# Kernel optimization log

Hardware: AMD Instinct MI355X
Metric: run time of the kernel (lower is better)

## Reference

```python
import jax, jax.numpy as jnp
import numpy as np

H, W, D, C = 32, 16, 16, 4
NUM_ITERS = 2
THETA_GAMMA = 3.0   # spatial (position-only) kernel bandwidth
THETA_ALPHA = 8.0   # bilateral position bandwidth
THETA_BETA = 0.5    # bilateral color bandwidth


def _attn(feats, q):
    # Gaussian-kernel attention: softmax_j(-0.5 * ||f_i - f_j||^2) @ q
    # feats: [N, F], q: [N, C] -> [N, C]
    sq = jnp.sum(feats * feats, axis=-1)
    logits = feats @ feats.T - 0.5 * (sq[:, None] + sq[None, :])  # [N, N]
    return jax.nn.softmax(logits, axis=-1) @ q


def setup_inputs() -> dict:
    key = jax.random.key(0)
    k1, k2 = jax.random.split(key)
    unaries = jax.random.normal(k1, (1, H, W, D, C), dtype=jnp.float32)
    rgb = jax.random.normal(k2, (1, H, W, D, 3), dtype=jnp.float32)
    eye = jnp.eye(C, dtype=jnp.float32)
    return {
        "unaries": unaries,
        "rgb": rgb,
        "spatial_ker_weights": eye,          # _diagonal_initializer
        "bilateral_ker_weights": eye,        # _diagonal_initializer
        "compatibility_matrix": -eye,        # _potts_model_initializer
    }


def reference(unaries, rgb, spatial_ker_weights, bilateral_ker_weights, compatibility_matrix):
    N = H * W * D
    # positions start at 1 as in tf.range(1, h+1)
    grids = jnp.meshgrid(jnp.arange(1, H + 1), jnp.arange(1, W + 1), jnp.arange(1, D + 1), indexing='ij')
    pos = jnp.stack(grids, axis=-1).astype(jnp.float32).reshape(N, 3)
    rgb_flat = rgb.reshape(N, 3)
    spatial_feats = pos / THETA_GAMMA                                             # [N, 3]
    bilateral_feats = jnp.concatenate([pos / THETA_ALPHA, rgb_flat / THETA_BETA], axis=-1)  # [N, 6]

    u = unaries.reshape(N, C)
    q = u
    for _ in range(NUM_ITERS):
        sm = jax.nn.softmax(q, axis=-1)                         # [N, C]
        spatial_out = _attn(spatial_feats, sm)                  # [N, C]
        bilateral_out = _attn(bilateral_feats, sm)              # [N, C]
        # message_passing = SK @ spatial + BK @ bilateral (class-space matmul)
        message = spatial_out @ spatial_ker_weights.T + bilateral_out @ bilateral_ker_weights.T
        pairwise = message @ compatibility_matrix.T             # [N, C]
        q = u + pairwise
    return q.reshape(unaries.shape)
```

## Files before the change

kernel.cpp:

```cpp
#include <hip/hip_runtime.h>


#define HH 32
#define WW 16
#define DDD 16
#define NN (HH * WW * DDD)
#define KS 16
#define JCH (NN / KS)
#define CONVB 32
#define ITILB (NN / 64)
#define GB2 (ITILB * KS)
#define L2E 1.4426950408889634f
#define C18 (L2E / 18.0f)
#define SQL2E 1.2011224087864498f
#define SB (SQL2E / 8.0f)
#define SC (SQL2E / 0.5f)

#if __has_builtin(__builtin_amdgcn_exp2f)
#define EXP2(x) __builtin_amdgcn_exp2f(x)
#else
#define EXP2(x) exp2f(x)
#endif

typedef __attribute__((ext_vector_type(8))) short bf16x8;
typedef __attribute__((ext_vector_type(4))) float f32x4;
#define MFMA16 __builtin_amdgcn_mfma_f32_16x16x32_bf16

__device__ __forceinline__ unsigned short f2bf(float x) {
    unsigned int u = __float_as_uint(x);
    return (unsigned short)((u + 0x7FFFu + ((u >> 16) & 1u)) >> 16);
}
__device__ __forceinline__ float bf2f(unsigned short b) {
    return __uint_as_float(((unsigned int)b) << 16);
}
__device__ __forceinline__ unsigned int pk(unsigned short a, unsigned short b) {
    return (unsigned int)a | ((unsigned int)b << 16);
}

__global__ __launch_bounds__(256) void prep(
    const float* __restrict__ u, const float* __restrict__ rgb,
    unsigned short* __restrict__ fq, unsigned short* __restrict__ fk,
    float* __restrict__ sm0, unsigned short* __restrict__ smT0)
{
    int i = blockIdx.x * 256 + threadIdx.x;
    int h = i >> 8, r = i & 255, w = r >> 4, d = r & 15;
    float f[6];
    f[0] = (float)(h + 1) * SB;
    f[1] = (float)(w + 1) * SB;
    f[2] = (float)(d + 1) * SB;
    f[3] = rgb[3 * i + 0] * SC;
    f[4] = rgb[3 * i + 1] * SC;
    f[5] = rgb[3 * i + 2] * SC;
    float nh = -0.5f * (f[0]*f[0] + f[1]*f[1] + f[2]*f[2] +
                        f[3]*f[3] + f[4]*f[4] + f[5]*f[5]);
    unsigned short hi[7], lo[7];
    #pragma unroll
    for (int k = 0; k < 6; ++k) {
        hi[k] = f2bf(f[k]);
        lo[k] = f2bf(f[k] - bf2f(hi[k]));
    }
    hi[6] = f2bf(nh);
    lo[6] = f2bf(nh - bf2f(hi[6]));
    const unsigned short one = 0x3F80;

    uint4* q4 = (uint4*)(fq + (size_t)i * 32);
    uint4* k4 = (uint4*)(fk + (size_t)i * 32);
    q4[0] = make_uint4(pk(hi[0],hi[1]), pk(hi[2],hi[3]), pk(hi[4],hi[5]), pk(hi[6],one));
    q4[1] = make_uint4(pk(lo[0],lo[1]), pk(lo[2],lo[3]), pk(lo[4],lo[5]), pk(lo[6],0));
    q4[2] = make_uint4(pk(hi[0],hi[1]), pk(hi[2],hi[3]), pk(hi[4],hi[5]), pk(0,one));
    q4[3] = make_uint4(0, 0, 0, 0);
    k4[0] = make_uint4(pk(hi[0],hi[1]), pk(hi[2],hi[3]), pk(hi[4],hi[5]), pk(one,hi[6]));
    k4[1] = make_uint4(pk(hi[0],hi[1]), pk(hi[2],hi[3]), pk(hi[4],hi[5]), pk(one,0));
    k4[2] = make_uint4(pk(lo[0],lo[1]), pk(lo[2],lo[3]), pk(lo[4],lo[5]), pk(0,lo[6]));
    k4[3] = make_uint4(0, 0, 0, 0);

    float4 q = ((const float4*)u)[i];
    float m = fmaxf(fmaxf(q.x, q.y), fmaxf(q.z, q.w));
    float e0 = EXP2((q.x - m) * L2E), e1 = EXP2((q.y - m) * L2E);
    float e2 = EXP2((q.z - m) * L2E), e3 = EXP2((q.w - m) * L2E);
    float rs = 1.0f / (e0 + e1 + e2 + e3);
    float s0 = e0 * rs, s1 = e1 * rs, s2 = e2 * rs, s3 = e3 * rs;
    ((float4*)sm0)[i] = make_float4(s0, s1, s2, s3);
    smT0[0 * NN + i] = f2bf(s0);
    smT0[1 * NN + i] = f2bf(s1);
    smT0[2 * NN + i] = f2bf(s2);
    smT0[3 * NN + i] = f2bf(s3);
}

__global__ __launch_bounds__(256, 8) void fused(
    const float* __restrict__ sm,
    const unsigned short* __restrict__ smT,
    const unsigned short* __restrict__ fq,
    const unsigned short* __restrict__ fk,
    float* __restrict__ part,
    float* __restrict__ tmp)
{
    __shared__ float lds[2048];
    int tid = threadIdx.x;

    if (blockIdx.x < GB2) {
        int b = blockIdx.x;
        int ibk = b >> 4;
        int kc = b & (KS - 1);
        int wv = tid >> 6, lane = tid & 63;
        int lm = lane & 15, lg = lane >> 4;
        int i0 = ibk * 64 + wv * 16;
        int j0 = kc * JCH;

        const bf16x8* FQ = (const bf16x8*)fq;
        const bf16x8* FK = (const bf16x8*)fk;
        bf16x8 Bf = FK[(size_t)(i0 + lm) * 4 + lg];
        const unsigned short* smc = smT + (size_t)(lm & 3) * NN;

        unsigned int* P = (unsigned int*)lds + wv * 320;
        f32x4 acc = {0.f, 0.f, 0.f, 0.f};
        const f32x4 zro = {0.f, 0.f, 0.f, 0.f};

        #pragma unroll 2
        for (int s = 0; s < JCH / 32; ++s) {
            int js = j0 + s * 32;
            bf16x8 A0 = FQ[(size_t)(js + lm) * 4 + lg];
            bf16x8 A1 = FQ[(size_t)(js + 16 + lm) * 4 + lg];
            f32x4 S0 = MFMA16(A0, Bf, zro, 0, 0, 0);
            f32x4 S1 = MFMA16(A1, Bf, zro, 0, 0, 0);
            uint2 w0, w1;
            w0.x = pk(f2bf(EXP2(S0[0])), f2bf(EXP2(S0[1])));
            w0.y = pk(f2bf(EXP2(S0[2])), f2bf(EXP2(S0[3])));
            w1.x = pk(f2bf(EXP2(S1[0])), f2bf(EXP2(S1[1])));
            w1.y = pk(f2bf(EXP2(S1[2])), f2bf(EXP2(S1[3])));
            *(uint2*)(P + lm * 20 + 2 * lg)     = w0;
            *(uint2*)(P + lm * 20 + 2 * lg + 8) = w1;
            bf16x8 Pf = *(const bf16x8*)(P + lm * 20 + 4 * lg);
            bf16x8 Sf = *(const bf16x8*)(smc + js + 8 * lg);
            acc = MFMA16(Pf, Sf, acc, 0, 0, 0);
        }
        if (lm < 4) {
            float* pp = part + (size_t)kc * (NN * 4);
            #pragma unroll
            for (int r = 0; r < 4; ++r)
                pp[(size_t)(i0 + 4 * lg + r) * 4 + lm] = acc[r];
        }
    } else {
        int h = blockIdx.x - GB2;
        int s = tid;
        int i = h * 256 + s;

        float* A = lds;
        float* B = lds + 1024;
        *((float4*)(A + 4 * s)) = ((const float4*)sm)[i];
        __syncthreads();

        int w = s >> 4, d = s & 15;
        float t0 = 0, t1 = 0, t2 = 0, t3 = 0;
        #pragma unroll
        for (int dp = 0; dp < DDD; ++dp) {
            float dd = (float)(d - dp);
            float k = EXP2(-dd * dd * C18);
            const float4 v = *((const float4*)(A + 4 * (w * 16 + dp)));
            t0 = fmaf(k, v.x, t0); t1 = fmaf(k, v.y, t1);
            t2 = fmaf(k, v.z, t2); t3 = fmaf(k, v.w, t3);
        }
        *((float4*)(B + 4 * s)) = make_float4(t0, t1, t2, t3);
        __syncthreads();

        float u0 = 0, u1 = 0, u2 = 0, u3 = 0;
        #pragma unroll
        for (int wp = 0; wp < WW; ++wp) {
            float dw = (float)(w - wp);
            float k = EXP2(-dw * dw * C18);
            const float4 v = *((const float4*)(B + 4 * (wp * 16 + d)));
            u0 = fmaf(k, v.x, u0); u1 = fmaf(k, v.y, u1);
            u2 = fmaf(k, v.z, u2); u3 = fmaf(k, v.w, u3);
        }
        *((float4*)(tmp + 4 * i)) = make_float4(u0, u1, u2, u3);
    }
}

__global__ __launch_bounds__(256) void reduce_finish(
    const float* __restrict__ part,
    const float* __restrict__ tmp,
    const float* __restrict__ u,
    const float* __restrict__ sk, const float* __restrict__ bk,
    const float* __restrict__ cm,
    float* __restrict__ qout,
    float* __restrict__ smout,
    unsigned short* __restrict__ smTout)
{
    int tid = threadIdx.x;
    int q = tid >> 6;
    int lane = tid & 63;
    int idx = blockIdx.x * 64 + lane;

    float bl = 0.0f;
    #pragma unroll
    for (int k = 0; k < KS / 4; ++k)
        bl += part[(size_t)(q * (KS / 4) + k) * (NN * 4) + idx];

    int i = idx >> 2;
    int h = i >> 8;
    int scid = idx & 1023;
    float sp = 0.0f;
    #pragma unroll
    for (int k = 0; k < 8; ++k) {
        int hp = q * 8 + k;
        float dh = (float)(h - hp);
        float kk = EXP2(-dh * dh * C18);
        sp = fmaf(kk, tmp[hp * 1024 + scid], sp);
    }

    __shared__ float Lb[4][64];
    __shared__ float Ls[4][64];
    Lb[q][lane] = bl;
    Ls[q][lane] = sp;
    __syncthreads();

    if (tid < 16) {
        float b4[4], s4[4];
        #pragma unroll
        for (int c = 0; c < 4; ++c) {
            int l = tid * 4 + c;
            b4[c] = Lb[0][l] + Lb[1][l] + Lb[2][l] + Lb[3][l];
            s4[c] = Ls[0][l] + Ls[1][l] + Ls[2][l] + Ls[3][l];
        }
        float rb = 1.0f / (b4[0] + b4[1] + b4[2] + b4[3]);
        float rs = 1.0f / (s4[0] + s4[1] + s4[2] + s4[3]);
        float bo[4], so[4];
        #pragma unroll
        for (int c = 0; c < 4; ++c) { bo[c] = b4[c] * rb; so[c] = s4[c] * rs; }
        float msg[4];
        #pragma unroll
        for (int c = 0; c < 4; ++c) {
            float m = 0.0f;
            #pragma unroll
            for (int d = 0; d < 4; ++d)
                m += sk[c * 4 + d] * so[d] + bk[c * 4 + d] * bo[d];
            msg[c] = m;
        }
        int ig = blockIdx.x * 16 + tid;
        float qv[4];
        #pragma unroll
        for (int c = 0; c < 4; ++c) {
            float pw = 0.0f;
            #pragma unroll
            for (int d = 0; d < 4; ++d) pw += cm[c * 4 + d] * msg[d];
            qv[c] = u[4 * ig + c] + pw;
        }
        *((float4*)(qout + 4 * ig)) = make_float4(qv[0], qv[1], qv[2], qv[3]);

        float mm = fmaxf(fmaxf(qv[0], qv[1]), fmaxf(qv[2], qv[3]));
        float e0 = EXP2((qv[0] - mm) * L2E), e1 = EXP2((qv[1] - mm) * L2E);
        float e2 = EXP2((qv[2] - mm) * L2E), e3 = EXP2((qv[3] - mm) * L2E);
        float er = 1.0f / (e0 + e1 + e2 + e3);
        float sv0 = e0 * er, sv1 = e1 * er, sv2 = e2 * er, sv3 = e3 * er;
        *((float4*)(smout + 4 * ig)) = make_float4(sv0, sv1, sv2, sv3);
        smTout[0 * NN + ig] = f2bf(sv0);
        smTout[1 * NN + ig] = f2bf(sv1);
        smTout[2 * NN + ig] = f2bf(sv2);
        smTout[3 * NN + ig] = f2bf(sv3);
    }
}

extern "C" void kernel_launch(void* const* d_in, const int* in_sizes, int n_in,
                              void* d_out, int out_size, void* d_ws, size_t ws_size,
                              hipStream_t stream)
{
    const float* u   = (const float*)d_in[0];
    const float* rgb = (const float*)d_in[1];
    const float* sk  = (const float*)d_in[2];
    const float* bk  = (const float*)d_in[3];
    const float* cm  = (const float*)d_in[4];
    float* out = (float*)d_out;

    float* part = (float*)d_ws;
    float* tmpP = part + (size_t)KS * NN * 4;
    float* smA  = tmpP + (size_t)NN * 4;
    float* smB  = smA  + (size_t)NN * 4;
    float* qbuf = smB  + (size_t)NN * 4;
    unsigned short* fq   = (unsigned short*)(qbuf + (size_t)NN * 4);
    unsigned short* fk   = fq + (size_t)NN * 32;
    unsigned short* smTA = fk + (size_t)NN * 32;
    unsigned short* smTB = smTA + (size_t)NN * 4;

    dim3 blk(256);
    dim3 gP(NN / 256);
    dim3 gF(GB2 + CONVB);
    dim3 gR(NN * 4 / 64);

    prep<<<gP, blk, 0, stream>>>(u, rgb, fq, fk, smA, smTA);
    fused<<<gF, blk, 0, stream>>>(smA, smTA, fq, fk, part, tmpP);
    reduce_finish<<<gR, blk, 0, stream>>>(part, tmpP, u, sk, bk, cm, qbuf, smB, smTB);
    fused<<<gF, blk, 0, stream>>>(smB, smTB, fq, fk, part, tmpP);
    reduce_finish<<<gR, blk, 0, stream>>>(part, tmpP, u, sk, bk, cm, out, smA, smTA);
}
```

Baseline: 76.82 us.

## Prefetch next j-tile operands, use packed bf16 convert, reorder conv blocks first

```diff
diff --git a/kernel.cpp b/kernel.cpp
--- a/kernel.cpp
+++ b/kernel.cpp
@@ -35,6 +35,11 @@
 }
 __device__ __forceinline__ unsigned int pk(unsigned short a, unsigned short b) {
     return (unsigned int)a | ((unsigned int)b << 16);
+}
+__device__ __forceinline__ unsigned int cvtpk(float lo, float hi) {
+    unsigned int r;
+    asm("v_cvt_pk_bf16_f32 %0, %1, %2" : "=v"(r) : "v"(lo), "v"(hi));
+    return r;
 }
 
 __global__ __launch_bounds__(256) void prep(
@@ -87,7 +92,7 @@
     smT0[3 * NN + i] = f2bf(s3);
 }
 
-__global__ __launch_bounds__(256, 8) void fused(
+__global__ __launch_bounds__(256, 4) void fused(
     const float* __restrict__ sm,
     const unsigned short* __restrict__ smT,
     const unsigned short* __restrict__ fq,
@@ -98,8 +103,8 @@
     __shared__ float lds[2048];
     int tid = threadIdx.x;
 
-    if (blockIdx.x < GB2) {
-        int b = blockIdx.x;
+    if (blockIdx.x >= CONVB) {
+        int b = blockIdx.x - CONVB;
         int ibk = b >> 4;
         int kc = b & (KS - 1);
         int wv = tid >> 6, lane = tid & 63;
@@ -116,23 +121,31 @@
         f32x4 acc = {0.f, 0.f, 0.f, 0.f};
         const f32x4 zro = {0.f, 0.f, 0.f, 0.f};
 
-        #pragma unroll 2
-        for (int s = 0; s < JCH / 32; ++s) {
+        const int NIT = JCH / 32;
+        bf16x8 A0 = FQ[(size_t)(j0 + lm) * 4 + lg];
+        bf16x8 A1 = FQ[(size_t)(j0 + 16 + lm) * 4 + lg];
+        bf16x8 Sf = *(const bf16x8*)(smc + j0 + 8 * lg);
+
+        for (int s = 0; s < NIT; ++s) {
             int js = j0 + s * 32;
-            bf16x8 A0 = FQ[(size_t)(js + lm) * 4 + lg];
-            bf16x8 A1 = FQ[(size_t)(js + 16 + lm) * 4 + lg];
+            bf16x8 A0n, A1n, Sfn;
+            if (s + 1 < NIT) {
+                A0n = FQ[(size_t)(js + 32 + lm) * 4 + lg];
+                A1n = FQ[(size_t)(js + 48 + lm) * 4 + lg];
+                Sfn = *(const bf16x8*)(smc + js + 32 + 8 * lg);
+            }
             f32x4 S0 = MFMA16(A0, Bf, zro, 0, 0, 0);
             f32x4 S1 = MFMA16(A1, Bf, zro, 0, 0, 0);
             uint2 w0, w1;
-            w0.x = pk(f2bf(EXP2(S0[0])), f2bf(EXP2(S0[1])));
-            w0.y = pk(f2bf(EXP2(S0[2])), f2bf(EXP2(S0[3])));
-            w1.x = pk(f2bf(EXP2(S1[0])), f2bf(EXP2(S1[1])));
-            w1.y = pk(f2bf(EXP2(S1[2])), f2bf(EXP2(S1[3])));
+            w0.x = cvtpk(EXP2(S0[0]), EXP2(S0[1]));
+            w0.y = cvtpk(EXP2(S0[2]), EXP2(S0[3]));
+            w1.x = cvtpk(EXP2(S1[0]), EXP2(S1[1]));
+            w1.y = cvtpk(EXP2(S1[2]), EXP2(S1[3]));
             *(uint2*)(P + lm * 20 + 2 * lg)     = w0;
             *(uint2*)(P + lm * 20 + 2 * lg + 8) = w1;
             bf16x8 Pf = *(const bf16x8*)(P + lm * 20 + 4 * lg);
-            bf16x8 Sf = *(const bf16x8*)(smc + js + 8 * lg);
             acc = MFMA16(Pf, Sf, acc, 0, 0, 0);
+            A0 = A0n; A1 = A1n; Sf = Sfn;
         }
         if (lm < 4) {
             float* pp = part + (size_t)kc * (NN * 4);
@@ -141,7 +154,7 @@
                 pp[(size_t)(i0 + 4 * lg + r) * 4 + lm] = acc[r];
         }
     } else {
-        int h = blockIdx.x - GB2;
+        int h = blockIdx.x;
         int s = tid;
         int i = h * 256 + s;
 
@@ -283,7 +296,7 @@
 
     dim3 blk(256);
     dim3 gP(NN / 256);
-    dim3 gF(GB2 + CONVB);
+    dim3 gF(CONVB + GB2);
     dim3 gR(NN * 4 / 64);
 
     prep<<<gP, blk, 0, stream>>>(u, rgb, fq, fk, smA, smTA);
```

Measured after the change: 82.80 us. +7.8%, slower.
